# Optimization experiments

Measured on AMD Instinct MI355X. Metric: run time of the kernel, lower is better.

## Reference

```python
import jax, jax.numpy as jnp
import numpy as np

B, T, E, H = 2, 2048, 2048, 16
D = E // H


def setup_inputs() -> dict:
    key = jax.random.key(0)
    ks = jax.random.split(key, 5)
    s = 0.02
    return {
        "x": jax.random.normal(ks[0], (B, T, E), jnp.float32),
        "Wq": jax.random.normal(ks[1], (E, E), jnp.float32) * s,
        "Wk": jax.random.normal(ks[2], (E, E), jnp.float32) * s,
        "Wv": jax.random.normal(ks[3], (E, E), jnp.float32) * s,
        "Wp": jax.random.normal(ks[4], (E, E), jnp.float32) * s,
        "bp": jnp.zeros((E,), jnp.float32),
    }


def reference(x, Wq, Wk, Wv, Wp, bp):
    b, t, e = x.shape
    h, d = H, E // H
    # torch Linear: y = x @ W.T (no bias for qkv)
    Q = (x @ Wq.T).reshape(b, h, t, d)  # faithful: view without transpose
    K = (x @ Wk.T).reshape(b, h, t, d)
    V = (x @ Wv.T).reshape(b, h, t, d)
    scores = jnp.einsum("bhqd,bhkd->bhqk", Q, K)
    causal = jnp.triu(jnp.ones((t, t), bool), k=1)  # True above diagonal
    scores = jnp.where(causal, -jnp.inf, scores)
    weights = jax.nn.softmax(scores / jnp.sqrt(jnp.float32(d)), axis=-1)
    # dropout p=0.0 (eval) -> identity
    ctx = jnp.einsum("bhqk,bhkd->bhqd", weights, V)  # (b,h,t,d)
    ctx = ctx.transpose(0, 2, 1, 3).reshape(b, t, e)
    return ctx @ Wp.T + bp
```

## Files before the change

kernel.cpp:

```cpp
#include <hip/hip_runtime.h>

#define SEQ   2048
#define EMB   2048
#define NHEAD 16
#define HDIM  128
#define ROWSM 4096

typedef float  f32x4   __attribute__((ext_vector_type(4)));
typedef float  f32x16  __attribute__((ext_vector_type(16)));
typedef __bf16 bf16x8  __attribute__((ext_vector_type(8)));

__device__ __forceinline__ unsigned short f2bf(float f) {
  union { float f; unsigned int u; } v; v.f = f;
  return (unsigned short)((v.u + 0x7fffu + ((v.u >> 16) & 1u)) >> 16);
}
__device__ __forceinline__ unsigned int pk2(float a, float b) {
  return (unsigned int)f2bf(a) | ((unsigned int)f2bf(b) << 16);
}

__device__ __forceinline__ void gload16(const void* g, void* l) {
  __builtin_amdgcn_global_load_lds(
      (__attribute__((address_space(1))) const unsigned int*)g,
      (__attribute__((address_space(3))) unsigned int*)l,
      16, 0, 0);
}

__global__ void cvt_bf16(const float* __restrict__ in,
                         unsigned short* __restrict__ out, int n4) {
  int i = blockIdx.x * 256 + threadIdx.x;
  if (i >= n4) return;
  float4 v = ((const float4*)in)[i];
  ushort4 o;
  o.x = f2bf(v.x); o.y = f2bf(v.y); o.z = f2bf(v.z); o.w = f2bf(v.w);
  ((ushort4*)out)[i] = o;
}

template <int STORE_F32>
__global__ __launch_bounds__(256, 2) void gemm_nt(
    const unsigned short* __restrict__ A, const unsigned short* __restrict__ B,
    void* __restrict__ Cout, const float* __restrict__ bias,
    int M, int N, int K) {
  __shared__ __align__(16) unsigned short As[128 * 64];
  __shared__ __align__(16) unsigned short Bs[128 * 64];
  const int tid  = threadIdx.x;
  const int lane = tid & 63;
  const int w    = tid >> 6;
  const int m0 = blockIdx.y * 128;
  const int n0 = blockIdx.x * 128;
  const int wm = (w >> 1) * 64;
  const int wn = (w & 1) * 64;
  const int lg = lane >> 4;
  const int lc = lane & 15;

  f32x4 acc[4][4] = {};

  const int srow = lane >> 3;
  const int scol = (lane & 7) * 8;

  for (int k0 = 0; k0 < K; k0 += 64) {
    if (k0) __syncthreads();
#pragma unroll
    for (int ii = 0; ii < 4; ++ii) {
      int i = w * 4 + ii;
      int r = i * 8 + srow;
      gload16(A + (size_t)(m0 + r) * K + k0 + scol, (char*)As + i * 1024);
      gload16(B + (size_t)(n0 + r) * K + k0 + scol, (char*)Bs + i * 1024);
    }
    __syncthreads();
#pragma unroll
    for (int kk = 0; kk < 2; ++kk) {
      const int co = kk * 32 + lg * 8;
      bf16x8 a[4], b[4];
#pragma unroll
      for (int i = 0; i < 4; ++i)
        a[i] = *(const bf16x8*)(As + (wm + i * 16 + lc) * 64 + co);
#pragma unroll
      for (int j = 0; j < 4; ++j)
        b[j] = *(const bf16x8*)(Bs + (wn + j * 16 + lc) * 64 + co);
#pragma unroll
      for (int i = 0; i < 4; ++i)
#pragma unroll
        for (int j = 0; j < 4; ++j)
          acc[i][j] = __builtin_amdgcn_mfma_f32_16x16x32_bf16(a[i], b[j], acc[i][j], 0, 0, 0);
    }
  }

  const int rb = lg * 4;
#pragma unroll
  for (int i = 0; i < 4; ++i) {
#pragma unroll
    for (int j = 0; j < 4; ++j) {
      int col = n0 + wn + j * 16 + lc;
#pragma unroll
      for (int r = 0; r < 4; ++r) {
        int row = m0 + wm + i * 16 + rb + r;
        if (STORE_F32) {
          ((float*)Cout)[(size_t)row * N + col] = acc[i][j][r] + bias[col];
        } else {
          ((unsigned short*)Cout)[(size_t)row * N + col] = f2bf(acc[i][j][r]);
        }
      }
    }
  }
}

__global__ __launch_bounds__(256, 2) void attn_causal(
    const unsigned short* __restrict__ Pq, const unsigned short* __restrict__ Pk,
    const unsigned short* __restrict__ Pv, unsigned short* __restrict__ ctx) {
  __shared__ __align__(16) unsigned short Ks[64 * 128];
  __shared__ __align__(16) unsigned short Vt[128 * 64];

  const int tid  = threadIdx.x;
  const int lane = tid & 63;
  const int w    = tid >> 6;
  const int ql   = lane & 31;
  const int hi   = lane >> 5;
  const int lg   = lane >> 4;
  const int lc   = lane & 15;

  const int bid = blockIdx.x;
  const int xcd = bid & 7;
  const int j   = bid >> 3;
  const int hh  = j >> 4;
  const int bh  = xcd * 4 + hh;
  const int b   = bh >> 4;
  const int h   = bh & 15;
  const int qtr = j & 15;
  const int qt  = (hh >= 2) ? (15 - qtr) : qtr;
  const int q0 = qt * 128;
  const int qw = q0 + w * 32;
  const int qg = qw + ql;

  const size_t hoff = (size_t)bh * SEQ * HDIM;
  const unsigned short* Q  = Pq + hoff;
  const unsigned short* Kh = Pk + hoff;
  const unsigned short* Vh = Pv + hoff;

  bf16x8 bq[8];
#pragma unroll
  for (int d8 = 0; d8 < 8; ++d8)
    bq[d8] = *(const bf16x8*)(Q + (size_t)qg * HDIM + d8 * 16 + hi * 8);

  const float NEG = -3.0e38f;
  f32x16 o[4];
#pragma unroll
  for (int dt = 0; dt < 4; ++dt)
#pragma unroll
    for (int r = 0; r < 16; ++r) o[dt][r] = 0.f;
  float m_r = NEG, l_r = 0.f;

  const float Cs   = 0.12753123161692858f;
  const float TDEF = 62.7f;

  const int ntiles = (q0 >> 6) + 2;
  for (int t = 0; t < ntiles; ++t) {
    const int kv0 = t * 64;
    if (t) __syncthreads();
#pragma unroll
    for (int ii = 0; ii < 4; ++ii) {
      int i = w * 4 + ii;
      int r = i * 4 + lg;
      int sd = lc ^ (r & 7);
      gload16(Kh + (size_t)(kv0 + r) * HDIM + sd * 8, (char*)Ks + i * 1024);
    }
#pragma unroll
    for (int uu = 0; uu < 2; ++uu) {
      int u = tid + uu * 256;
      int kp = u >> 4, dg = u & 15;
      int k = kp * 2, d0 = dg * 8;
      uint4 r0 = *(const uint4*)(Vh + (size_t)(kv0 + k) * HDIM + d0);
      uint4 r1 = *(const uint4*)(Vh + (size_t)(kv0 + k + 1) * HDIM + d0);
      const unsigned short* e0 = (const unsigned short*)&r0;
      const unsigned short* e1 = (const unsigned short*)&r1;
#pragma unroll
      for (int jj = 0; jj < 8; ++jj) {
        int d = d0 + jj;
        int slotswz = (k >> 3) ^ jj ^ (dg & 7);
        int byteoff = d * 128 + (slotswz << 4) + (k & 7) * 2;
        *(unsigned int*)((char*)Vt + byteoff) =
            (unsigned int)e0[jj] | ((unsigned int)e1[jj] << 16);
      }
    }
    __syncthreads();

    if (kv0 > qw + 31) continue;
    const bool s1on = (kv0 + 32 <= qw + 31);
    const bool diag = (kv0 + 63 > qw);

    f32x16 c0, c1;
#pragma unroll
    for (int r = 0; r < 16; ++r) { c0[r] = 0.f; c1[r] = s1on ? 0.f : NEG; }
#pragma unroll
    for (int d8 = 0; d8 < 8; ++d8) {
      bf16x8 ak = *(const bf16x8*)((const char*)Ks + ql * 256 +
                                   (((d8 * 2 + hi) ^ (ql & 7)) << 4));
      c0 = __builtin_amdgcn_mfma_f32_32x32x16_bf16(ak, bq[d8], c0, 0, 0, 0);
    }
    if (s1on) {
#pragma unroll
      for (int d8 = 0; d8 < 8; ++d8) {
        bf16x8 ak = *(const bf16x8*)((const char*)Ks + (32 + ql) * 256 +
                                     (((d8 * 2 + hi) ^ (ql & 7)) << 4));
        c1 = __builtin_amdgcn_mfma_f32_32x32x16_bf16(ak, bq[d8], c1, 0, 0, 0);
      }
    }
    if (diag) {
#pragma unroll
      for (int r = 0; r < 16; ++r) {
        int kvl = (r & 3) + 8 * (r >> 2) + 4 * hi;
        if (kv0 + kvl > qg) c0[r] = NEG;
        if (s1on && kv0 + 32 + kvl > qg) c1[r] = NEG;
      }
    }
    float rm = c0[0];
#pragma unroll
    for (int r = 1; r < 16; ++r) rm = fmaxf(rm, c0[r]);
#pragma unroll
    for (int r = 0; r < 16; ++r) rm = fmaxf(rm, c1[r]);
    rm = fmaxf(rm, __shfl_xor(rm, 32));

    if (__any(rm > m_r + TDEF)) {
      float mnew = fmaxf(m_r, rm);
      float alpha = exp2f((m_r - mnew) * Cs);
      m_r = mnew;
      l_r *= alpha;
#pragma unroll
      for (int r = 0; r < 16; ++r) {
        float ar = __shfl(alpha, (r & 3) + 8 * (r >> 2) + 4 * hi);
#pragma unroll
        for (int dt = 0; dt < 4; ++dt) o[dt][r] *= ar;
      }
    }
#pragma unroll
    for (int r = 0; r < 16; ++r) {
      c0[r] = exp2f((c0[r] - m_r) * Cs);
      c1[r] = exp2f((c1[r] - m_r) * Cs);
    }
    float ps = 0.f;
#pragma unroll
    for (int r = 0; r < 16; ++r) ps += c0[r] + c1[r];
    ps += __shfl_xor(ps, 32);
    l_r += ps;

    bf16x8 pa[4];
#pragma unroll
    for (int t4 = 0; t4 < 4; ++t4) {
      const f32x16& cc = (t4 < 2) ? c0 : c1;
      const int rA = (t4 & 1) * 8;
      unsigned int pkL0 = pk2(cc[rA + 0], cc[rA + 1]);
      unsigned int pkL1 = pk2(cc[rA + 2], cc[rA + 3]);
      unsigned int pkH0 = pk2(cc[rA + 4], cc[rA + 5]);
      unsigned int pkH1 = pk2(cc[rA + 6], cc[rA + 7]);
      unsigned int give0 = hi ? pkL0 : pkH0;
      unsigned int give1 = hi ? pkL1 : pkH1;
      unsigned int keep0 = hi ? pkH0 : pkL0;
      unsigned int keep1 = hi ? pkH1 : pkL1;
      unsigned int recv0 = __shfl_xor(give0, 32);
      unsigned int recv1 = __shfl_xor(give1, 32);
      union { unsigned int u[4]; bf16x8 v; } pu;
      pu.u[0] = hi ? recv0 : keep0;
      pu.u[1] = hi ? recv1 : keep1;
      pu.u[2] = hi ? keep0 : recv0;
      pu.u[3] = hi ? keep1 : recv1;
      pa[t4] = pu.v;
    }
#pragma unroll
    for (int t4 = 0; t4 < 4; ++t4) {
      if (diag && kv0 + t4 * 16 > qw + 31) continue;
#pragma unroll
      for (int dt = 0; dt < 4; ++dt) {
        int d = dt * 32 + ql;
        bf16x8 bv = *(const bf16x8*)((const char*)Vt + d * 128 +
                                     (((t4 * 2 + hi) ^ (d & 7) ^ ((d >> 3) & 7)) << 4));
        o[dt] = __builtin_amdgcn_mfma_f32_32x32x16_bf16(pa[t4], bv, o[dt], 0, 0, 0);
      }
    }
  }

  float linv = 1.0f / l_r;
  unsigned short* outp = ctx + (size_t)b * SEQ * EMB + (size_t)h * HDIM;
#pragma unroll
  for (int r = 0; r < 16; ++r) {
    int kvl = (r & 3) + 8 * (r >> 2) + 4 * hi;
    float lr = __shfl(linv, kvl);
    int qrow = qw + kvl;
#pragma unroll
    for (int dt = 0; dt < 4; ++dt)
      outp[(size_t)qrow * EMB + dt * 32 + ql] = f2bf(o[dt][r] * lr);
  }
}

extern "C" void kernel_launch(void* const* d_in, const int* in_sizes, int n_in,
                              void* d_out, int out_size, void* d_ws, size_t ws_size,
                              hipStream_t stream) {
  const float* x  = (const float*)d_in[0];
  const float* Wq = (const float*)d_in[1];
  const float* Wk = (const float*)d_in[2];
  const float* Wv = (const float*)d_in[3];
  const float* Wp = (const float*)d_in[4];
  const float* bp = (const float*)d_in[5];

  char* ws = (char*)d_ws;
  unsigned short* xb = (unsigned short*)ws;
  unsigned short* Wb = (unsigned short*)(ws + (size_t)(16u << 20));
  unsigned short* Pq = (unsigned short*)(ws + (size_t)(24u << 20));
  unsigned short* Pk = (unsigned short*)(ws + (size_t)(40u << 20));
  unsigned short* Pv = (unsigned short*)(ws + (size_t)(56u << 20));

  const int nX4 = ROWSM * EMB / 4;
  const int nW4 = EMB * EMB / 4;

  cvt_bf16<<<nX4 / 256, 256, 0, stream>>>(x, xb, nX4);

  dim3 ggrid(EMB / 128, ROWSM / 128);

  cvt_bf16<<<nW4 / 256, 256, 0, stream>>>(Wq, Wb, nW4);
  gemm_nt<0><<<ggrid, 256, 0, stream>>>(xb, Wb, Pq, nullptr, ROWSM, EMB, EMB);
  cvt_bf16<<<nW4 / 256, 256, 0, stream>>>(Wk, Wb, nW4);
  gemm_nt<0><<<ggrid, 256, 0, stream>>>(xb, Wb, Pk, nullptr, ROWSM, EMB, EMB);
  cvt_bf16<<<nW4 / 256, 256, 0, stream>>>(Wv, Wb, nW4);
  gemm_nt<0><<<ggrid, 256, 0, stream>>>(xb, Wb, Pv, nullptr, ROWSM, EMB, EMB);

  attn_causal<<<512, 256, 0, stream>>>(Pq, Pk, Pv, xb);

  cvt_bf16<<<nW4 / 256, 256, 0, stream>>>(Wp, Wb, nW4);
  gemm_nt<1><<<ggrid, 256, 0, stream>>>(xb, Wb, d_out, bp, ROWSM, EMB, EMB);
}
```

Before: 302.4 us.

## Batch QKV projections into one launch and widen attention KV tiles to 128

The three weight conversions become one launch, and the three QKV GEMMs become a single grid with z=3. Converted Wk/Wv are staged temporarily in the output buffer. Pq/Pk/Pv are written contiguously at stride ROWSM*EMB, which matches the existing workspace offsets. The attention kernel now loads 128-row K/V tiles, which halves barrier count at the cost of doubled LDS (64KB), and it adds s_setprio around the MFMA sections. Larger LDS may cut occupancy, and the unroll-1 loops may add overhead.

```diff
diff --git a/kernel.cpp b/kernel.cpp
--- a/kernel.cpp
+++ b/kernel.cpp
@@ -35,11 +35,88 @@
   ((ushort4*)out)[i] = o;
 }
 
-template <int STORE_F32>
-__global__ __launch_bounds__(256, 2) void gemm_nt(
+__global__ void cvt_bf16_3(const float* __restrict__ i0, const float* __restrict__ i1,
+                           const float* __restrict__ i2, unsigned short* __restrict__ o0,
+                           unsigned short* __restrict__ o1, unsigned short* __restrict__ o2,
+                           int n4) {
+  const float* in = (blockIdx.z == 0) ? i0 : (blockIdx.z == 1) ? i1 : i2;
+  unsigned short* out = (blockIdx.z == 0) ? o0 : (blockIdx.z == 1) ? o1 : o2;
+  int i = blockIdx.x * 256 + threadIdx.x;
+  if (i >= n4) return;
+  float4 v = ((const float4*)in)[i];
+  ushort4 o;
+  o.x = f2bf(v.x); o.y = f2bf(v.y); o.z = f2bf(v.z); o.w = f2bf(v.w);
+  ((ushort4*)out)[i] = o;
+}
+
+__global__ __launch_bounds__(256, 2) void gemm_qkv(
+    const unsigned short* __restrict__ A,
+    const unsigned short* __restrict__ B0, const unsigned short* __restrict__ B1,
+    const unsigned short* __restrict__ B2, unsigned short* __restrict__ Cbase) {
+  __shared__ __align__(16) unsigned short As[128 * 64];
+  __shared__ __align__(16) unsigned short Bs[128 * 64];
+  const unsigned short* Bm = (blockIdx.z == 0) ? B0 : (blockIdx.z == 1) ? B1 : B2;
+  unsigned short* C = Cbase + (size_t)blockIdx.z * ROWSM * EMB;
+
+  const int tid  = threadIdx.x;
+  const int lane = tid & 63;
+  const int w    = tid >> 6;
+  const int m0 = blockIdx.y * 128;
+  const int n0 = blockIdx.x * 128;
+  const int wm = (w >> 1) * 64;
+  const int wn = (w & 1) * 64;
+  const int lg = lane >> 4;
+  const int lc = lane & 15;
+
+  f32x4 acc[4][4] = {};
+  const int srow = lane >> 3;
+  const int scol = (lane & 7) * 8;
+
+  for (int k0 = 0; k0 < EMB; k0 += 64) {
+    if (k0) __syncthreads();
+#pragma unroll
+    for (int ii = 0; ii < 4; ++ii) {
+      int i = w * 4 + ii;
+      int r = i * 8 + srow;
+      gload16(A  + (size_t)(m0 + r) * EMB + k0 + scol, (char*)As + i * 1024);
+      gload16(Bm + (size_t)(n0 + r) * EMB + k0 + scol, (char*)Bs + i * 1024);
+    }
+    __syncthreads();
+#pragma unroll
+    for (int kk = 0; kk < 2; ++kk) {
+      const int co = kk * 32 + lg * 8;
+      bf16x8 a[4], b[4];
+#pragma unroll
+      for (int i = 0; i < 4; ++i)
+        a[i] = *(const bf16x8*)(As + (wm + i * 16 + lc) * 64 + co);
+#pragma unroll
+      for (int j = 0; j < 4; ++j)
+        b[j] = *(const bf16x8*)(Bs + (wn + j * 16 + lc) * 64 + co);
+#pragma unroll
+      for (int i = 0; i < 4; ++i)
+#pragma unroll
+        for (int j = 0; j < 4; ++j)
+          acc[i][j] = __builtin_amdgcn_mfma_f32_16x16x32_bf16(a[i], b[j], acc[i][j], 0, 0, 0);
+    }
+  }
+
+  const int rb = lg * 4;
+#pragma unroll
+  for (int i = 0; i < 4; ++i)
+#pragma unroll
+    for (int j = 0; j < 4; ++j) {
+      int col = n0 + wn + j * 16 + lc;
+#pragma unroll
+      for (int r = 0; r < 4; ++r) {
+        int row = m0 + wm + i * 16 + rb + r;
+        C[(size_t)row * EMB + col] = f2bf(acc[i][j][r]);
+      }
+    }
+}
+
+__global__ __launch_bounds__(256, 2) void gemm_p(
     const unsigned short* __restrict__ A, const unsigned short* __restrict__ B,
-    void* __restrict__ Cout, const float* __restrict__ bias,
-    int M, int N, int K) {
+    float* __restrict__ Cout, const float* __restrict__ bias) {
   __shared__ __align__(16) unsigned short As[128 * 64];
   __shared__ __align__(16) unsigned short Bs[128 * 64];
   const int tid  = threadIdx.x;
@@ -53,18 +130,17 @@
   const int lc = lane & 15;
 
   f32x4 acc[4][4] = {};
-
   const int srow = lane >> 3;
   const int scol = (lane & 7) * 8;
 
-  for (int k0 = 0; k0 < K; k0 += 64) {
+  for (int k0 = 0; k0 < EMB; k0 += 64) {
     if (k0) __syncthreads();
 #pragma unroll
     for (int ii = 0; ii < 4; ++ii) {
       int i = w * 4 + ii;
       int r = i * 8 + srow;
-      gload16(A + (size_t)(m0 + r) * K + k0 + scol, (char*)As + i * 1024);
-      gload16(B + (size_t)(n0 + r) * K + k0 + scol, (char*)Bs + i * 1024);
+      gload16(A + (size_t)(m0 + r) * EMB + k0 + scol, (char*)As + i * 1024);
+      gload16(B + (size_t)(n0 + r) * EMB + k0 + scol, (char*)Bs + i * 1024);
     }
     __syncthreads();
 #pragma unroll
@@ -87,28 +163,23 @@
 
   const int rb = lg * 4;
 #pragma unroll
-  for (int i = 0; i < 4; ++i) {
+  for (int i = 0; i < 4; ++i)
 #pragma unroll
     for (int j = 0; j < 4; ++j) {
       int col = n0 + wn + j * 16 + lc;
 #pragma unroll
       for (int r = 0; r < 4; ++r) {
         int row = m0 + wm + i * 16 + rb + r;
-        if (STORE_F32) {
-          ((float*)Cout)[(size_t)row * N + col] = acc[i][j][r] + bias[col];
-        } else {
-          ((unsigned short*)Cout)[(size_t)row * N + col] = f2bf(acc[i][j][r]);
-        }
-      }
-    }
-  }
+        Cout[(size_t)row * EMB + col] = acc[i][j][r] + bias[col];
+      }
+    }
 }
 
 __global__ __launch_bounds__(256, 2) void attn_causal(
     const unsigned short* __restrict__ Pq, const unsigned short* __restrict__ Pk,
     const unsigned short* __restrict__ Pv, unsigned short* __restrict__ ctx) {
-  __shared__ __align__(16) unsigned short Ks[64 * 128];
-  __shared__ __align__(16) unsigned short Vt[128 * 64];
+  __shared__ __align__(16) unsigned short Ks[128 * 128];
+  __shared__ __align__(16) unsigned short Vt[128 * 128];
 
   const int tid  = threadIdx.x;
   const int lane = tid & 63;
@@ -120,12 +191,12 @@
 
   const int bid = blockIdx.x;
   const int xcd = bid & 7;
-  const int j   = bid >> 3;
-  const int hh  = j >> 4;
+  const int jj_ = bid >> 3;
+  const int hh  = jj_ >> 4;
   const int bh  = xcd * 4 + hh;
   const int b   = bh >> 4;
   const int h   = bh & 15;
-  const int qtr = j & 15;
+  const int qtr = jj_ & 15;
   const int qt  = (hh >= 2) ? (15 - qtr) : qtr;
   const int q0 = qt * 128;
   const int qw = q0 + w * 32;
@@ -152,128 +223,149 @@
   const float Cs   = 0.12753123161692858f;
   const float TDEF = 62.7f;
 
-  const int ntiles = (q0 >> 6) + 2;
-  for (int t = 0; t < ntiles; ++t) {
-    const int kv0 = t * 64;
-    if (t) __syncthreads();
-#pragma unroll
-    for (int ii = 0; ii < 4; ++ii) {
-      int i = w * 4 + ii;
+  const int nt128 = qt + 1;
+  for (int tt = 0; tt < nt128; ++tt) {
+    const int kv0 = tt * 128;
+    if (tt) __syncthreads();
+#pragma unroll
+    for (int ii = 0; ii < 8; ++ii) {
+      int i = w * 8 + ii;
       int r = i * 4 + lg;
       int sd = lc ^ (r & 7);
       gload16(Kh + (size_t)(kv0 + r) * HDIM + sd * 8, (char*)Ks + i * 1024);
     }
-#pragma unroll
-    for (int uu = 0; uu < 2; ++uu) {
-      int u = tid + uu * 256;
-      int kp = u >> 4, dg = u & 15;
-      int k = kp * 2, d0 = dg * 8;
-      uint4 r0 = *(const uint4*)(Vh + (size_t)(kv0 + k) * HDIM + d0);
-      uint4 r1 = *(const uint4*)(Vh + (size_t)(kv0 + k + 1) * HDIM + d0);
-      const unsigned short* e0 = (const unsigned short*)&r0;
-      const unsigned short* e1 = (const unsigned short*)&r1;
-#pragma unroll
-      for (int jj = 0; jj < 8; ++jj) {
-        int d = d0 + jj;
-        int slotswz = (k >> 3) ^ jj ^ (dg & 7);
-        int byteoff = d * 128 + (slotswz << 4) + (k & 7) * 2;
-        *(unsigned int*)((char*)Vt + byteoff) =
-            (unsigned int)e0[jj] | ((unsigned int)e1[jj] << 16);
+#pragma unroll 1
+    for (int hv = 0; hv < 2; ++hv) {
+      uint4 vr[4];
+      const unsigned short* Vs = Vh + (size_t)(kv0 + hv * 64) * HDIM;
+#pragma unroll
+      for (int uu = 0; uu < 2; ++uu) {
+        int u = tid + uu * 256;
+        int kp = u >> 4, dg = u & 15;
+        int k = kp * 2, d0 = dg * 8;
+        vr[uu * 2]     = *(const uint4*)(Vs + (size_t)k * HDIM + d0);
+        vr[uu * 2 + 1] = *(const uint4*)(Vs + (size_t)(k + 1) * HDIM + d0);
+      }
+#pragma unroll
+      for (int uu = 0; uu < 2; ++uu) {
+        int u = tid + uu * 256;
+        int kp = u >> 4, dg = u & 15;
+        int k = kp * 2, d0 = dg * 8;
+        const unsigned short* e0 = (const unsigned short*)&vr[uu * 2];
+        const unsigned short* e1 = (const unsigned short*)&vr[uu * 2 + 1];
+#pragma unroll
+        for (int jj = 0; jj < 8; ++jj) {
+          int d = d0 + jj;
+          int slot = ((hv << 3) | (k >> 3)) ^ jj ^ (dg & 7);
+          int byteoff = d * 256 + (slot << 4) + (k & 7) * 2;
+          *(unsigned int*)((char*)Vt + byteoff) =
+              (unsigned int)e0[jj] | ((unsigned int)e1[jj] << 16);
+        }
       }
     }
     __syncthreads();
 
-    if (kv0 > qw + 31) continue;
-    const bool s1on = (kv0 + 32 <= qw + 31);
-    const bool diag = (kv0 + 63 > qw);
-
-    f32x16 c0, c1;
-#pragma unroll
-    for (int r = 0; r < 16; ++r) { c0[r] = 0.f; c1[r] = s1on ? 0.f : NEG; }
-#pragma unroll
-    for (int d8 = 0; d8 < 8; ++d8) {
-      bf16x8 ak = *(const bf16x8*)((const char*)Ks + ql * 256 +
-                                   (((d8 * 2 + hi) ^ (ql & 7)) << 4));
-      c0 = __builtin_amdgcn_mfma_f32_32x32x16_bf16(ak, bq[d8], c0, 0, 0, 0);
-    }
-    if (s1on) {
+#pragma unroll 1
+    for (int hf = 0; hf < 2; ++hf) {
+      const int kv0h = kv0 + hf * 64;
+      if (kv0h > qw + 31) continue;
+      const bool s1on = (kv0h + 32 <= qw + 31);
+      const bool diag = (kv0h + 63 > qw);
+      const char* ksb = (const char*)Ks + hf * 64 * 256;
+
+      f32x16 c0, c1;
+#pragma unroll
+      for (int r = 0; r < 16; ++r) { c0[r] = 0.f; c1[r] = s1on ? 0.f : NEG; }
+      __builtin_amdgcn_s_setprio(1);
 #pragma unroll
       for (int d8 = 0; d8 < 8; ++d8) {
-        bf16x8 ak = *(const bf16x8*)((const char*)Ks + (32 + ql) * 256 +
+        bf16x8 ak = *(const bf16x8*)(ksb + ql * 256 +
                                      (((d8 * 2 + hi) ^ (ql & 7)) << 4));
-        c1 = __builtin_amdgcn_mfma_f32_32x32x16_bf16(ak, bq[d8], c1, 0, 0, 0);
-      }
-    }
-    if (diag) {
+        c0 = __builtin_amdgcn_mfma_f32_32x32x16_bf16(ak, bq[d8], c0, 0, 0, 0);
+      }
+      if (s1on) {
+#pragma unroll
+        for (int d8 = 0; d8 < 8; ++d8) {
+          bf16x8 ak = *(const bf16x8*)(ksb + (32 + ql) * 256 +
+                                       (((d8 * 2 + hi) ^ (ql & 7)) << 4));
+          c1 = __builtin_amdgcn_mfma_f32_32x32x16_bf16(ak, bq[d8], c1, 0, 0, 0);
+        }
+      }
+      __builtin_amdgcn_s_setprio(0);
+
+      if (diag) {
+#pragma unroll
+        for (int r = 0; r < 16; ++r) {
+          int kvl = (r & 3) + 8 * (r >> 2) + 4 * hi;
+          if (kv0h + kvl > qg) c0[r] = NEG;
+          if (s1on && kv0h + 32 + kvl > qg) c1[r] = NEG;
+        }
+      }
+      float rm = c0[0];
+#pragma unroll
+      for (int r = 1; r < 16; ++r) rm = fmaxf(rm, c0[r]);
+#pragma unroll
+      for (int r = 0; r < 16; ++r) rm = fmaxf(rm, c1[r]);
+      rm = fmaxf(rm, __shfl_xor(rm, 32));
+
+      if (__any(rm > m_r + TDEF)) {
+        float mnew = fmaxf(m_r, rm);
+        float alpha = exp2f((m_r - mnew) * Cs);
+        m_r = mnew;
+        l_r *= alpha;
+#pragma unroll
+        for (int r = 0; r < 16; ++r) {
+          float ar = __shfl(alpha, (r & 3) + 8 * (r >> 2) + 4 * hi);
+#pragma unroll
+          for (int dt = 0; dt < 4; ++dt) o[dt][r] *= ar;
+        }
+      }
 #pragma unroll
       for (int r = 0; r < 16; ++r) {
-        int kvl = (r & 3) + 8 * (r >> 2) + 4 * hi;
-        if (kv0 + kvl > qg) c0[r] = NEG;
-        if (s1on && kv0 + 32 + kvl > qg) c1[r] = NEG;
-      }
-    }
-    float rm = c0[0];
-#pragma unroll
-    for (int r = 1; r < 16; ++r) rm = fmaxf(rm, c0[r]);
-#pragma unroll
-    for (int r = 0; r < 16; ++r) rm = fmaxf(rm, c1[r]);
-    rm = fmaxf(rm, __shfl_xor(rm, 32));
-
-    if (__any(rm > m_r + TDEF)) {
-      float mnew = fmaxf(m_r, rm);
-      float alpha = exp2f((m_r - mnew) * Cs);
-      m_r = mnew;
-      l_r *= alpha;
-#pragma unroll
-      for (int r = 0; r < 16; ++r) {
-        float ar = __shfl(alpha, (r & 3) + 8 * (r >> 2) + 4 * hi);
-#pragma unroll
-        for (int dt = 0; dt < 4; ++dt) o[dt][r] *= ar;
-      }
-    }
-#pragma unroll
-    for (int r = 0; r < 16; ++r) {
-      c0[r] = exp2f((c0[r] - m_r) * Cs);
-      c1[r] = exp2f((c1[r] - m_r) * Cs);
-    }
-    float ps = 0.f;
-#pragma unroll
-    for (int r = 0; r < 16; ++r) ps += c0[r] + c1[r];
-    ps += __shfl_xor(ps, 32);
-    l_r += ps;
-
-    bf16x8 pa[4];
-#pragma unroll
-    for (int t4 = 0; t4 < 4; ++t4) {
-      const f32x16& cc = (t4 < 2) ? c0 : c1;
-      const int rA = (t4 & 1) * 8;
-      unsigned int pkL0 = pk2(cc[rA + 0], cc[rA + 1]);
-      unsigned int pkL1 = pk2(cc[rA + 2], cc[rA + 3]);
-      unsigned int pkH0 = pk2(cc[rA + 4], cc[rA + 5]);
-      unsigned int pkH1 = pk2(cc[rA + 6], cc[rA + 7]);
-      unsigned int give0 = hi ? pkL0 : pkH0;
-      unsigned int give1 = hi ? pkL1 : pkH1;
-      unsigned int keep0 = hi ? pkH0 : pkL0;
-      unsigned int keep1 = hi ? pkH1 : pkL1;
-      unsigned int recv0 = __shfl_xor(give0, 32);
-      unsigned int recv1 = __shfl_xor(give1, 32);
-      union { unsigned int u[4]; bf16x8 v; } pu;
-      pu.u[0] = hi ? recv0 : keep0;
-      pu.u[1] = hi ? recv1 : keep1;
-      pu.u[2] = hi ? keep0 : recv0;
-      pu.u[3] = hi ? keep1 : recv1;
-      pa[t4] = pu.v;
-    }
-#pragma unroll
-    for (int t4 = 0; t4 < 4; ++t4) {
-      if (diag && kv0 + t4 * 16 > qw + 31) continue;
-#pragma unroll
-      for (int dt = 0; dt < 4; ++dt) {
-        int d = dt * 32 + ql;
-        bf16x8 bv = *(const bf16x8*)((const char*)Vt + d * 128 +
-                                     (((t4 * 2 + hi) ^ (d & 7) ^ ((d >> 3) & 7)) << 4));
-        o[dt] = __builtin_amdgcn_mfma_f32_32x32x16_bf16(pa[t4], bv, o[dt], 0, 0, 0);
-      }
+        c0[r] = exp2f((c0[r] - m_r) * Cs);
+        c1[r] = exp2f((c1[r] - m_r) * Cs);
+      }
+      float ps = 0.f;
+#pragma unroll
+      for (int r = 0; r < 16; ++r) ps += c0[r] + c1[r];
+      ps += __shfl_xor(ps, 32);
+      l_r += ps;
+
+      bf16x8 pa[4];
+#pragma unroll
+      for (int t4 = 0; t4 < 4; ++t4) {
+        const f32x16& cc = (t4 < 2) ? c0 : c1;
+        const int rA = (t4 & 1) * 8;
+        unsigned int pkL0 = pk2(cc[rA + 0], cc[rA + 1]);
+        unsigned int pkL1 = pk2(cc[rA + 2], cc[rA + 3]);
+        unsigned int pkH0 = pk2(cc[rA + 4], cc[rA + 5]);
+        unsigned int pkH1 = pk2(cc[rA + 6], cc[rA + 7]);
+        unsigned int give0 = hi ? pkL0 : pkH0;
+        unsigned int give1 = hi ? pkL1 : pkH1;
+        unsigned int keep0 = hi ? pkH0 : pkL0;
+        unsigned int keep1 = hi ? pkH1 : pkL1;
+        unsigned int recv0 = __shfl_xor(give0, 32);
+        unsigned int recv1 = __shfl_xor(give1, 32);
+        union { unsigned int u[4]; bf16x8 v; } pu;
+        pu.u[0] = hi ? recv0 : keep0;
+        pu.u[1] = hi ? recv1 : keep1;
+        pu.u[2] = hi ? keep0 : recv0;
+        pu.u[3] = hi ? keep1 : recv1;
+        pa[t4] = pu.v;
+      }
+      __builtin_amdgcn_s_setprio(1);
+#pragma unroll
+      for (int t4 = 0; t4 < 4; ++t4) {
+        if (diag && kv0h + t4 * 16 > qw + 31) continue;
+#pragma unroll
+        for (int dt = 0; dt < 4; ++dt) {
+          int d = dt * 32 + ql;
+          int slot = ((hf << 3) | (t4 << 1) | hi) ^ (d & 7) ^ ((d >> 3) & 7);
+          bf16x8 bv = *(const bf16x8*)((const char*)Vt + d * 256 + (slot << 4));
+          o[dt] = __builtin_amdgcn_mfma_f32_32x32x16_bf16(pa[t4], bv, o[dt], 0, 0, 0);
+        }
+      }
+      __builtin_amdgcn_s_setprio(0);
     }
   }
 
@@ -306,23 +398,19 @@
   unsigned short* Pq = (unsigned short*)(ws + (size_t)(24u << 20));
   unsigned short* Pk = (unsigned short*)(ws + (size_t)(40u << 20));
   unsigned short* Pv = (unsigned short*)(ws + (size_t)(56u << 20));
+  unsigned short* WvS = (unsigned short*)d_out;
+  unsigned short* WkS = (unsigned short*)d_out + (size_t)4 * 1024 * 1024;
 
   const int nX4 = ROWSM * EMB / 4;
   const int nW4 = EMB * EMB / 4;
 
   cvt_bf16<<<nX4 / 256, 256, 0, stream>>>(x, xb, nX4);
-
-  dim3 ggrid(EMB / 128, ROWSM / 128);
-
-  cvt_bf16<<<nW4 / 256, 256, 0, stream>>>(Wq, Wb, nW4);
-  gemm_nt<0><<<ggrid, 256, 0, stream>>>(xb, Wb, Pq, nullptr, ROWSM, EMB, EMB);
-  cvt_bf16<<<nW4 / 256, 256, 0, stream>>>(Wk, Wb, nW4);
-  gemm_nt<0><<<ggrid, 256, 0, stream>>>(xb, Wb, Pk, nullptr, ROWSM, EMB, EMB);
-  cvt_bf16<<<nW4 / 256, 256, 0, stream>>>(Wv, Wb, nW4);
-  gemm_nt<0><<<ggrid, 256, 0, stream>>>(xb, Wb, Pv, nullptr, ROWSM, EMB, EMB);
+  cvt_bf16_3<<<dim3(nW4 / 256, 1, 3), 256, 0, stream>>>(Wq, Wk, Wv, Wb, WkS, WvS, nW4);
+
+  gemm_qkv<<<dim3(EMB / 128, ROWSM / 128, 3), 256, 0, stream>>>(xb, Wb, WkS, WvS, Pq);
 
   attn_causal<<<512, 256, 0, stream>>>(Pq, Pk, Pv, xb);
 
   cvt_bf16<<<nW4 / 256, 256, 0, stream>>>(Wp, Wb, nW4);
-  gemm_nt<1><<<ggrid, 256, 0, stream>>>(xb, Wb, d_out, bp, ROWSM, EMB, EMB);
-}
+  gemm_p<<<dim3(EMB / 128, ROWSM / 128), 256, 0, stream>>>(xb, Wb, (float*)d_out, bp);
+}
```

Result: faster. 286.8 us (-5.2%).
